# Kernel tuning notes

Measured on AMD Instinct MI355X. Metric: run time of the kernel, lower is better.

## Reference

```python
import jax, jax.numpy as jnp
import numpy as np

B, T, D, U = 32, 4096, 256, 256


def setup_inputs() -> dict:
    key = jax.random.key(0)
    ks = jax.random.split(key, 5)
    s = 1.0 / np.sqrt(D)
    return {
        "query": jax.random.normal(ks[0], (B, D), jnp.float32),
        "values": jax.random.normal(ks[1], (B, T, D), jnp.float32),
        "W1": jax.random.normal(ks[2], (D, U), jnp.float32) * s,
        "b1": jnp.zeros((U,), jnp.float32),
        "W2": jax.random.normal(ks[3], (D, U), jnp.float32) * s,
        "b2": jnp.zeros((U,), jnp.float32),
        "V": jax.random.normal(ks[4], (U, 1), jnp.float32) * (1.0 / np.sqrt(U)),
        "bV": jnp.zeros((1,), jnp.float32),
    }


def reference(query, values, W1, b1, W2, b2, V, bV):
    # score[b,t,u] = tanh(values @ W1 + b1 + (query @ W2 + b2)[:,None,:])
    proj_v = jnp.einsum("btd,du->btu", values, W1) + b1        # [B,T,U]
    proj_q = (query @ W2 + b2)[:, None, :]                      # [B,1,U]
    score = jnp.tanh(proj_v + proj_q) @ V + bV                  # [B,T,1]
    attn = jax.nn.softmax(score, axis=1)                        # softmax over T
    context = jnp.sum(attn * values, axis=1)                    # [B,D]
    return (context, attn)
```

## Files before the change

kernel.cpp:

```cpp
#include <hip/hip_runtime.h>
#include <hip/hip_bf16.h>

typedef __attribute__((ext_vector_type(4))) float f32x4;
typedef __attribute__((ext_vector_type(8))) short s16x8;

static constexpr int Bn = 32;
static constexpr int Tn = 4096;
static constexpr int Dn = 256;
static constexpr int Un = 256;
static constexpr int CTX_C = 16;

__device__ __forceinline__ ushort f2bf(float f) {
    unsigned x = __float_as_uint(f);
    x += 0x7fffu + ((x >> 16) & 1u);
    return (ushort)(x >> 16);
}

__device__ __forceinline__ float fast_tanh(float x) {
    float ax = fabsf(x);
    float e = __expf(-2.0f * ax);
    float r = __fdividef(1.0f - e, 1.0f + e);
    return copysignf(r, x);
}

__device__ __forceinline__ void gload_lds16(const void* g, void* l) {
    __builtin_amdgcn_global_load_lds(
        (const __attribute__((address_space(1))) unsigned*)g,
        (__attribute__((address_space(3))) unsigned*)l, 16, 0, 0);
}

__global__ __launch_bounds__(256) void k_w1t(const float* __restrict__ W1,
                                             ushort* __restrict__ W1T) {
    const int u = blockIdx.x, d = threadIdx.x;
    W1T[u * Dn + d] = f2bf(W1[d * Un + u]);
}

__global__ __launch_bounds__(256) void k_qproj(const float* __restrict__ query,
                                               const float* __restrict__ W2,
                                               const float* __restrict__ b1,
                                               const float* __restrict__ b2,
                                               float* __restrict__ qb) {
    __shared__ float qs[Dn];
    const int b = blockIdx.x, u = threadIdx.x;
    qs[u] = query[b * Dn + u];
    __syncthreads();
    float acc = b1[u] + b2[u];
    #pragma unroll 8
    for (int d = 0; d < Dn; ++d) acc += qs[d] * W2[d * Un + u];
    qb[b * Un + u] = acc;
}

__global__ __launch_bounds__(256, 2) void k_score(const float* __restrict__ values,
                                                  const ushort* __restrict__ W1T,
                                                  const float* __restrict__ qb,
                                                  const float* __restrict__ Vw,
                                                  const float* __restrict__ bV,
                                                  float* __restrict__ scores) {
    __shared__ __align__(16) ushort Al[64][264];
    __shared__ __align__(16) ushort Bl[256][32];
    const int tid = threadIdx.x;
    const int b = blockIdx.y;
    const int t0 = blockIdx.x * 64;
    const int wid = tid >> 6;
    const int lane = tid & 63;
    const int l15 = lane & 15;
    const int hi = lane >> 4;

    float Vreg[16], qreg[16];
    #pragma unroll
    for (int ut = 0; ut < 16; ++ut) {
        int u = ut * 16 + l15;
        Vreg[ut] = Vw[u];
        qreg[ut] = qb[b * Un + u];
    }

    const float* vbase = values + ((size_t)b * Tn + t0) * Dn;
    #pragma unroll
    for (int i = 0; i < 8; ++i) {
        int flat = i * 2048 + tid * 8;
        int row = flat >> 8, col = flat & 255;
        const float4 f0 = *(const float4*)&vbase[row * Dn + col];
        const float4 f1 = *(const float4*)&vbase[row * Dn + col + 4];
        s16x8 p;
        p[0] = (short)f2bf(f0.x); p[1] = (short)f2bf(f0.y);
        p[2] = (short)f2bf(f0.z); p[3] = (short)f2bf(f0.w);
        p[4] = (short)f2bf(f1.x); p[5] = (short)f2bf(f1.y);
        p[6] = (short)f2bf(f1.z); p[7] = (short)f2bf(f1.w);
        *(s16x8*)&Al[row][col] = p;
    }

    f32x4 acc[16];
    #pragma unroll
    for (int ut = 0; ut < 16; ++ut) acc[ut] = (f32x4){0.f, 0.f, 0.f, 0.f};

    for (int kc = 0; kc < 8; ++kc) {
        const int k0 = kc * 32;
        #pragma unroll
        for (int j = 0; j < 4; ++j) {
            int flat = j * 256 + tid;
            const ushort* gsrc = W1T + (flat >> 2) * Dn + k0 + (flat & 3) * 8;
            ushort* ldst = &Bl[0][0] + (size_t)(j * 256 + (tid & ~63)) * 8;
            gload_lds16(gsrc, ldst);
        }
        __syncthreads();

        const s16x8 af = *(const s16x8*)&Al[wid * 16 + l15][k0 + hi * 8];
        #pragma unroll
        for (int ut = 0; ut < 16; ++ut) {
            const s16x8 bf = *(const s16x8*)&Bl[ut * 16 + l15][hi * 8];
            acc[ut] = __builtin_amdgcn_mfma_f32_16x16x32_bf16(af, bf, acc[ut], 0, 0, 0);
        }
        __syncthreads();
    }

    float ps[4] = {0.f, 0.f, 0.f, 0.f};
    #pragma unroll
    for (int ut = 0; ut < 16; ++ut) {
        #pragma unroll
        for (int i = 0; i < 4; ++i)
            ps[i] += fast_tanh(acc[ut][i] + qreg[ut]) * Vreg[ut];
    }
    const float bv = bV[0];
    #pragma unroll
    for (int i = 0; i < 4; ++i) {
        ps[i] += __shfl_xor(ps[i], 1, 64);
        ps[i] += __shfl_xor(ps[i], 2, 64);
        ps[i] += __shfl_xor(ps[i], 4, 64);
        ps[i] += __shfl_xor(ps[i], 8, 64);
        if (l15 == 0) scores[b * Tn + t0 + wid * 16 + hi * 4 + i] = ps[i] + bv;
    }
}

__global__ __launch_bounds__(256) void k_softmax(const float* __restrict__ scores,
                                                 float* __restrict__ attn) {
    const int b = blockIdx.x, tid = threadIdx.x;
    __shared__ float redm[4];
    __shared__ float reds[4];
    float s[16];
    float m = -1e30f;
    #pragma unroll
    for (int k = 0; k < 16; ++k) {
        s[k] = scores[b * Tn + k * 256 + tid];
        m = fmaxf(m, s[k]);
    }
    #pragma unroll
    for (int off = 32; off > 0; off >>= 1) m = fmaxf(m, __shfl_xor(m, off, 64));
    const int wid = tid >> 6;
    if ((tid & 63) == 0) redm[wid] = m;
    __syncthreads();
    m = fmaxf(fmaxf(redm[0], redm[1]), fmaxf(redm[2], redm[3]));
    float sum = 0.f;
    #pragma unroll
    for (int k = 0; k < 16; ++k) { s[k] = __expf(s[k] - m); sum += s[k]; }
    #pragma unroll
    for (int off = 32; off > 0; off >>= 1) sum += __shfl_xor(sum, off, 64);
    if ((tid & 63) == 0) reds[wid] = sum;
    __syncthreads();
    sum = reds[0] + reds[1] + reds[2] + reds[3];
    const float inv = 1.0f / sum;
    #pragma unroll
    for (int k = 0; k < 16; ++k) attn[b * Tn + k * 256 + tid] = s[k] * inv;
}

__global__ __launch_bounds__(256) void k_ctx_partial(const float* __restrict__ values,
                                                     const float* __restrict__ attn,
                                                     float* __restrict__ partial) {
    const int c = blockIdx.x, b = blockIdx.y, tid = threadIdx.x;
    const int d4 = (tid & 63) * 4, tg = tid >> 6;
    float4 a = make_float4(0.f, 0.f, 0.f, 0.f);
    const float* vbase = values + (size_t)b * Tn * Dn;
    const int tstart = c * (Tn / CTX_C);
    for (int t = tstart + tg; t < tstart + Tn / CTX_C; t += 4) {
        const float w = attn[b * Tn + t];
        const float4 v = *(const float4*)&vbase[(size_t)t * Dn + d4];
        a.x += w * v.x; a.y += w * v.y; a.z += w * v.z; a.w += w * v.w;
    }
    __shared__ float4 red[4][64];
    red[tg][tid & 63] = a;
    __syncthreads();
    if (tg == 0) {
        const float4 r0 = red[0][tid], r1 = red[1][tid], r2 = red[2][tid], r3 = red[3][tid];
        a.x = r0.x + r1.x + r2.x + r3.x;
        a.y = r0.y + r1.y + r2.y + r3.y;
        a.z = r0.z + r1.z + r2.z + r3.z;
        a.w = r0.w + r1.w + r2.w + r3.w;
        *(float4*)&partial[((size_t)b * CTX_C + c) * Dn + d4] = a;
    }
}

__global__ __launch_bounds__(256) void k_ctx_final(const float* __restrict__ partial,
                                                   float* __restrict__ context) {
    const int b = blockIdx.x, d = threadIdx.x;
    float a = 0.f;
    #pragma unroll
    for (int c = 0; c < CTX_C; ++c) a += partial[((size_t)b * CTX_C + c) * Dn + d];
    context[b * Dn + d] = a;
}

extern "C" void kernel_launch(void* const* d_in, const int* in_sizes, int n_in,
                              void* d_out, int out_size, void* d_ws, size_t ws_size,
                              hipStream_t stream) {
    const float* query  = (const float*)d_in[0];
    const float* values = (const float*)d_in[1];
    const float* W1     = (const float*)d_in[2];
    const float* b1     = (const float*)d_in[3];
    const float* W2     = (const float*)d_in[4];
    const float* b2     = (const float*)d_in[5];
    const float* Vw     = (const float*)d_in[6];
    const float* bV     = (const float*)d_in[7];

    float* context = (float*)d_out;
    float* attn    = (float*)d_out + Bn * Dn;
    float*  partial = (float*)d_ws;
    float*  qb      = partial + Bn * CTX_C * Dn;
    ushort* W1T     = (ushort*)(qb + Bn * Un);

    k_w1t<<<dim3(Un), dim3(Dn), 0, stream>>>(W1, W1T);
    k_qproj<<<dim3(Bn), dim3(256), 0, stream>>>(query, W2, b1, b2, qb);
    k_score<<<dim3(Tn / 64, Bn), dim3(256), 0, stream>>>(values, W1T, qb, Vw, bV, attn);
    k_softmax<<<dim3(Bn), dim3(256), 0, stream>>>(attn, attn);
    k_ctx_partial<<<dim3(CTX_C, Bn), dim3(256), 0, stream>>>(values, attn, partial);
    k_ctx_final<<<dim3(Bn), dim3(256), 0, stream>>>(partial, context);
}
```

Baseline: 95.55 us.

## Retile score GEMM by U per wave, double-buffer and swizzle W1 LDS tiles

Each wave in the score kernel now owns 64 U columns across all 64 T rows, instead of 16 T rows across all 256 U. This cuts per-wave B-fragment LDS reads, so each A and B fragment feeds 4 MFMAs. W1T chunks are double-buffered in LDS so the global-to-LDS load of the next K chunk overlaps the current MFMAs, and the B tile uses an XOR swizzle to reduce bank conflicts. Per-wave partial scores are then reduced across waves through shared memory, which adds one barrier and a little more LDS.

```diff
diff --git a/kernel.cpp b/kernel.cpp
--- a/kernel.cpp
+++ b/kernel.cpp
@@ -57,7 +57,8 @@
                                                   const float* __restrict__ bV,
                                                   float* __restrict__ scores) {
     __shared__ __align__(16) ushort Al[64][264];
-    __shared__ __align__(16) ushort Bl[256][32];
+    __shared__ __align__(16) ushort Bl[2][256][32];
+    __shared__ float sred[4][64];
     const int tid = threadIdx.x;
     const int b = blockIdx.y;
     const int t0 = blockIdx.x * 64;
@@ -65,11 +66,12 @@
     const int lane = tid & 63;
     const int l15 = lane & 15;
     const int hi = lane >> 4;
-
-    float Vreg[16], qreg[16];
-    #pragma unroll
-    for (int ut = 0; ut < 16; ++ut) {
-        int u = ut * 16 + l15;
+    const int swz = hi ^ ((l15 >> 1) & 3);
+
+    float Vreg[4], qreg[4];
+    #pragma unroll
+    for (int ut = 0; ut < 4; ++ut) {
+        int u = wid * 64 + ut * 16 + l15;
         Vreg[ut] = Vw[u];
         qreg[ut] = qb[b * Un + u];
     }
@@ -89,45 +91,76 @@
         *(s16x8*)&Al[row][col] = p;
     }
 
-    f32x4 acc[16];
-    #pragma unroll
-    for (int ut = 0; ut < 16; ++ut) acc[ut] = (f32x4){0.f, 0.f, 0.f, 0.f};
-
-    for (int kc = 0; kc < 8; ++kc) {
-        const int k0 = kc * 32;
+    auto stage_b = [&](int kc, int buf) {
         #pragma unroll
         for (int j = 0; j < 4; ++j) {
-            int flat = j * 256 + tid;
-            const ushort* gsrc = W1T + (flat >> 2) * Dn + k0 + (flat & 3) * 8;
-            ushort* ldst = &Bl[0][0] + (size_t)(j * 256 + (tid & ~63)) * 8;
+            int f = j * 256 + tid;
+            int u = f >> 2, cs = f & 3;
+            int cd = cs ^ ((u >> 1) & 3);
+            const ushort* gsrc = W1T + u * Dn + kc * 32 + cd * 8;
+            ushort* ldst = &Bl[buf][0][0] + (size_t)(j * 256 + (tid & ~63)) * 8;
             gload_lds16(gsrc, ldst);
         }
+    };
+
+    stage_b(0, 0);
+
+    f32x4 acc[4][4];
+    #pragma unroll
+    for (int tt = 0; tt < 4; ++tt)
+        #pragma unroll
+        for (int ut = 0; ut < 4; ++ut) acc[tt][ut] = (f32x4){0.f, 0.f, 0.f, 0.f};
+
+    __syncthreads();
+
+    int cur = 0;
+    for (int kc = 0; kc < 8; ++kc) {
+        if (kc < 7) stage_b(kc + 1, cur ^ 1);
+        const int k0 = kc * 32;
+        s16x8 af[4], bfm[4];
+        #pragma unroll
+        for (int tt = 0; tt < 4; ++tt)
+            af[tt] = *(const s16x8*)&Al[tt * 16 + l15][k0 + hi * 8];
+        #pragma unroll
+        for (int ut = 0; ut < 4; ++ut)
+            bfm[ut] = *(const s16x8*)&Bl[cur][wid * 64 + ut * 16 + l15][swz * 8];
+        #pragma unroll
+        for (int tt = 0; tt < 4; ++tt)
+            #pragma unroll
+            for (int ut = 0; ut < 4; ++ut)
+                acc[tt][ut] = __builtin_amdgcn_mfma_f32_16x16x32_bf16(af[tt], bfm[ut], acc[tt][ut], 0, 0, 0);
         __syncthreads();
-
-        const s16x8 af = *(const s16x8*)&Al[wid * 16 + l15][k0 + hi * 8];
-        #pragma unroll
-        for (int ut = 0; ut < 16; ++ut) {
-            const s16x8 bf = *(const s16x8*)&Bl[ut * 16 + l15][hi * 8];
-            acc[ut] = __builtin_amdgcn_mfma_f32_16x16x32_bf16(af, bf, acc[ut], 0, 0, 0);
+        cur ^= 1;
+    }
+
+    float ps[4][4];
+    #pragma unroll
+    for (int tt = 0; tt < 4; ++tt)
+        #pragma unroll
+        for (int i = 0; i < 4; ++i) ps[tt][i] = 0.f;
+    #pragma unroll
+    for (int tt = 0; tt < 4; ++tt)
+        #pragma unroll
+        for (int ut = 0; ut < 4; ++ut)
+            #pragma unroll
+            for (int i = 0; i < 4; ++i)
+                ps[tt][i] += fast_tanh(acc[tt][ut][i] + qreg[ut]) * Vreg[ut];
+
+    #pragma unroll
+    for (int tt = 0; tt < 4; ++tt)
+        #pragma unroll
+        for (int i = 0; i < 4; ++i) {
+            float v = ps[tt][i];
+            v += __shfl_xor(v, 1, 64);
+            v += __shfl_xor(v, 2, 64);
+            v += __shfl_xor(v, 4, 64);
+            v += __shfl_xor(v, 8, 64);
+            if (l15 == 0) sred[wid][tt * 16 + hi * 4 + i] = v;
         }
-        __syncthreads();
-    }
-
-    float ps[4] = {0.f, 0.f, 0.f, 0.f};
-    #pragma unroll
-    for (int ut = 0; ut < 16; ++ut) {
-        #pragma unroll
-        for (int i = 0; i < 4; ++i)
-            ps[i] += fast_tanh(acc[ut][i] + qreg[ut]) * Vreg[ut];
-    }
-    const float bv = bV[0];
-    #pragma unroll
-    for (int i = 0; i < 4; ++i) {
-        ps[i] += __shfl_xor(ps[i], 1, 64);
-        ps[i] += __shfl_xor(ps[i], 2, 64);
-        ps[i] += __shfl_xor(ps[i], 4, 64);
-        ps[i] += __shfl_xor(ps[i], 8, 64);
-        if (l15 == 0) scores[b * Tn + t0 + wid * 16 + hi * 4 + i] = ps[i] + bv;
+    __syncthreads();
+    if (tid < 64) {
+        float s = sred[0][tid] + sred[1][tid] + sred[2][tid] + sred[3][tid] + bV[0];
+        scores[b * Tn + t0 + tid] = s;
     }
 }
 
```

Result: slower. 101.8 us (+6.6%).
